# Kernel optimization log

Hardware: AMD Instinct MI355X
Metric: run time of the kernel (lower is better)

The kernel has to match this reference:

```python
import jax, jax.numpy as jnp
import numpy as np

N_NODES = 100000
N_EDGES = 1250000
D_IN = 64
D_OUT = 64


def setup_inputs() -> dict:
    key = jax.random.key(0)
    k_h, k_e, k_src, k_dst, k_w, k_b = jax.random.split(key, 6)
    h = jax.random.normal(k_h, (N_NODES, D_IN), dtype=jnp.float32)
    e = jax.random.normal(k_e, (N_EDGES, 1), dtype=jnp.float32)
    src = jax.random.randint(k_src, (N_EDGES,), 0, N_NODES, dtype=jnp.int64)
    dst = jax.random.randint(k_dst, (N_EDGES,), 0, N_NODES, dtype=jnp.int64)
    W = jax.random.normal(k_w, (D_OUT, D_IN), dtype=jnp.float32) / np.sqrt(D_IN)
    b = jax.random.normal(k_b, (D_OUT,), dtype=jnp.float32) * 0.01
    return {"h": h, "e": e, "src": src, "dst": dst, "W": W, "b": b}


def reference(h, e, src, dst, W, b):
    # u_mul_e: gather source node features and multiply by edge features [E,1] -> [E,D]
    m = h[src] * e
    # fn.sum('m','ft'): scatter-add messages into destination nodes -> [N,D]
    ft = jax.ops.segment_sum(m, dst, num_segments=N_NODES)
    # nn.Linear(input_dim, output_dim)
    return ft @ W.T + b
```

## Files before the change

kernel.cpp:

```cpp
#include <hip/hip_runtime.h>

#define N_NODES 100000
#define N_EDGES 1250000
#define D 64
#define BUCKET_BITS 6
#define BUCKET_SZ 64
#define NBUCK 1563
#define CAP 1024
#define EPT 8
#define EPB (EPT * 256)
#define BIN_BLOCKS ((N_EDGES + EPB - 1) / EPB)


typedef __attribute__((ext_vector_type(8))) short bf16x8;
typedef __attribute__((ext_vector_type(4))) float f32x4;

__device__ __forceinline__ unsigned bf16_rne(float x) {
    unsigned u = __float_as_uint(x);
    return (u + 0x7FFFu + ((u >> 16) & 1u)) >> 16;
}
__device__ __forceinline__ float bf16_to_f(unsigned short v) {
    return __uint_as_float(((unsigned)v) << 16);
}

__device__ __forceinline__ void bf16_split(float x, short& hi, short& lo) {
    unsigned hb = bf16_rne(x);
    float fh = __uint_as_float(hb << 16);
    hi = (short)hb;
    lo = (short)bf16_rne(x - fh);
}

__global__ __launch_bounds__(256) void transform_kernel(const float* __restrict__ h,
                                                        const float* __restrict__ W,
                                                        unsigned short* __restrict__ g16) {
    int t = threadIdx.x;
    int lane = t & 63;
    int w = t >> 6;
    int li = lane & 15;
    int lg = lane >> 4;
    int nodebase = blockIdx.x * 64 + w * 16;

    bf16x8 bhi[4][2], blo[4][2];
#pragma unroll
    for (int nt = 0; nt < 4; ++nt) {
#pragma unroll
        for (int kk = 0; kk < 2; ++kk) {
            const float* wp = W + (nt * 16 + li) * D + kk * 32 + lg * 8;
            float4 w0 = *(const float4*)wp;
            float4 w1 = *(const float4*)(wp + 4);
            float v[8] = {w0.x, w0.y, w0.z, w0.w, w1.x, w1.y, w1.z, w1.w};
            bf16x8 h8, l8;
#pragma unroll
            for (int e = 0; e < 8; ++e) { short a, b; bf16_split(v[e], a, b); h8[e] = a; l8[e] = b; }
            bhi[nt][kk] = h8;
            blo[nt][kk] = l8;
        }
    }

    int arow = nodebase + li;
    if (arow > N_NODES - 1) arow = N_NODES - 1;
    bf16x8 ahi[2], alo[2];
#pragma unroll
    for (int kk = 0; kk < 2; ++kk) {
        const float* hp = h + (long)arow * D + kk * 32 + lg * 8;
        float4 h0 = *(const float4*)hp;
        float4 h1 = *(const float4*)(hp + 4);
        float v[8] = {h0.x, h0.y, h0.z, h0.w, h1.x, h1.y, h1.z, h1.w};
        bf16x8 h8, l8;
#pragma unroll
        for (int e = 0; e < 8; ++e) { short a, b; bf16_split(v[e], a, b); h8[e] = a; l8[e] = b; }
        ahi[kk] = h8;
        alo[kk] = l8;
    }

    f32x4 acc[4];
#pragma unroll
    for (int nt = 0; nt < 4; ++nt) acc[nt] = (f32x4){0.f, 0.f, 0.f, 0.f};
#pragma unroll
    for (int kk = 0; kk < 2; ++kk) {
#pragma unroll
        for (int nt = 0; nt < 4; ++nt) {
            acc[nt] = __builtin_amdgcn_mfma_f32_16x16x32_bf16(ahi[kk], bhi[nt][kk], acc[nt], 0, 0, 0);
            acc[nt] = __builtin_amdgcn_mfma_f32_16x16x32_bf16(ahi[kk], blo[nt][kk], acc[nt], 0, 0, 0);
            acc[nt] = __builtin_amdgcn_mfma_f32_16x16x32_bf16(alo[kk], bhi[nt][kk], acc[nt], 0, 0, 0);
        }
    }

#pragma unroll
    for (int nt = 0; nt < 4; ++nt) {
#pragma unroll
        for (int r = 0; r < 4; ++r) {
            int n = nodebase + lg * 4 + r;
            if (n < N_NODES) g16[(long)n * D + nt * 16 + li] = (unsigned short)bf16_rne(acc[nt][r]);
        }
    }
}

__global__ __launch_bounds__(256) void bin_edges_kernel(const int* __restrict__ src,
                                                        const int* __restrict__ dst,
                                                        const float* __restrict__ e,
                                                        int* __restrict__ gcursor,
                                                        int2* __restrict__ packed) {
    __shared__ int lhist[NBUCK];
    int t = threadIdx.x;
    for (int j = t; j < NBUCK; j += 256) lhist[j] = 0;
    __syncthreads();

    int b[EPT], r[EPT], sv[EPT];
    float ev[EPT];
    int base = blockIdx.x * EPB;
#pragma unroll
    for (int j = 0; j < EPT; ++j) {
        int i = base + j * 256 + t;
        b[j] = -1;
        if (i < N_EDGES) {
            int d = dst[i];
            b[j] = d >> BUCKET_BITS;
            sv[j] = src[i] | ((d & (BUCKET_SZ - 1)) << 20);
            ev[j] = e[i];
            r[j] = atomicAdd(&lhist[b[j]], 1);
        }
    }
    __syncthreads();

    for (int x = t; x < NBUCK; x += 256) {
        int c = lhist[x];
        lhist[x] = (c > 0) ? atomicAdd(&gcursor[x], c) : 0;
    }
    __syncthreads();

#pragma unroll
    for (int j = 0; j < EPT; ++j) {
        if (b[j] >= 0) {
            int pos = lhist[b[j]] + r[j];
            if (pos < CAP) packed[b[j] * CAP + pos] = make_int2(sv[j], __float_as_int(ev[j]));
        }
    }
}

__global__ __launch_bounds__(256) void gather_bucket_kernel(const unsigned short* __restrict__ g16,
                                                            const int2* __restrict__ packed,
                                                            const int* __restrict__ gcursor,
                                                            const float* __restrict__ bias,
                                                            float* __restrict__ out) {
    __shared__ int2 eds[CAP];
    __shared__ int nhist[BUCKET_SZ];
    __shared__ int nbase[BUCKET_SZ];
    __shared__ int ncur[BUCKET_SZ];
    __shared__ int tmp[BUCKET_SZ];

    int t = threadIdx.x;
    int bk = blockIdx.x;
    int start = bk * CAP;
    int cnt = gcursor[bk];
    if (cnt > CAP) cnt = CAP;

    if (t < BUCKET_SZ) nhist[t] = 0;
    __syncthreads();

    for (int i = t; i < cnt; i += 256) {
        int2 p = packed[start + i];
        atomicAdd(&nhist[(p.x >> 20) & (BUCKET_SZ - 1)], 1);
    }
    __syncthreads();

    if (t < BUCKET_SZ) tmp[t] = nhist[t];
    __syncthreads();
#pragma unroll
    for (int off = 1; off < BUCKET_SZ; off <<= 1) {
        int x = 0;
        if (t < BUCKET_SZ && t >= off) x = tmp[t - off];
        __syncthreads();
        if (t < BUCKET_SZ) tmp[t] += x;
        __syncthreads();
    }
    if (t < BUCKET_SZ) {
        int s = tmp[t] - nhist[t];
        nbase[t] = s;
        ncur[t] = s;
    }
    __syncthreads();

    for (int i = t; i < cnt; i += 256) {
        int2 p = packed[start + i];
        int dl = (p.x >> 20) & (BUCKET_SZ - 1);
        int pos = atomicAdd(&ncur[dl], 1);
        eds[pos] = p;
    }
    __syncthreads();

    int w = t >> 6;
    int lane = t & 63;
    float bv = bias[lane];
    for (int jj = 0; jj < 16; ++jj) {
        int n = w * 16 + jj;
        int gn = bk * BUCKET_SZ + n;
        int s = nbase[n];
        int c = nhist[n];
        float acc = bv;
        int k = 0;
        for (; k + 4 <= c; k += 4) {
            int2 p0 = eds[s + k];
            int2 p1 = eds[s + k + 1];
            int2 p2 = eds[s + k + 2];
            int2 p3 = eds[s + k + 3];
            float g0 = bf16_to_f(g16[(p0.x & 0xFFFFF) * D + lane]);
            float g1 = bf16_to_f(g16[(p1.x & 0xFFFFF) * D + lane]);
            float g2 = bf16_to_f(g16[(p2.x & 0xFFFFF) * D + lane]);
            float g3 = bf16_to_f(g16[(p3.x & 0xFFFFF) * D + lane]);
            acc += __int_as_float(p0.y) * g0;
            acc += __int_as_float(p1.y) * g1;
            acc += __int_as_float(p2.y) * g2;
            acc += __int_as_float(p3.y) * g3;
        }
        for (; k < c; ++k) {
            int2 p = eds[s + k];
            acc += __int_as_float(p.y) * bf16_to_f(g16[(p.x & 0xFFFFF) * D + lane]);
        }
        if (gn < N_NODES) out[gn * D + lane] = acc;
    }
}

extern "C" void kernel_launch(void* const* d_in, const int* in_sizes, int n_in,
                              void* d_out, int out_size, void* d_ws, size_t ws_size,
                              hipStream_t stream) {
    const float* h   = (const float*)d_in[0];
    const float* e   = (const float*)d_in[1];
    const int*   src = (const int*)d_in[2];
    const int*   dst = (const int*)d_in[3];
    const float* W   = (const float*)d_in[4];
    const float* b   = (const float*)d_in[5];
    float* out = (float*)d_out;

    char* ws = (char*)d_ws;
    int2*           packed  = (int2*)          (ws);
    int*            gcursor = (int*)           (ws + 12804096);
    unsigned short* g16     = (unsigned short*)(ws + 12810368);

    transform_kernel<<<(N_NODES + 63) / 64, 256, 0, stream>>>(h, W, g16);

    hipMemsetAsync(gcursor, 0, NBUCK * sizeof(int), stream);
    bin_edges_kernel<<<BIN_BLOCKS, 256, 0, stream>>>(src, dst, e, gcursor, packed);

    gather_bucket_kernel<<<NBUCK, 256, 0, stream>>>(g16, packed, gcursor, b, out);
}
```

Before: 174.9 us.

## Replace per-bucket local sort with shared-memory atomic accumulation in gather

The gather kernel no longer counts, prefix-scans and reorders each bucket's edges in shared memory. Each wave now takes a contiguous quarter of the bucket's edges and atomically adds the weighted messages into a 64x64 shared accumulator, which removes several block-wide barriers and passes over the packed edges. The changeset also folds the gcursor memset into the transform kernel, stages the transform output through shared memory so it is written as 16-byte stores, and doubles the edges per thread in the binning kernel. The cost is contention on LDS float atomics and a summation order that is no longer deterministic.

```diff
diff --git a/kernel.cpp b/kernel.cpp
--- a/kernel.cpp
+++ b/kernel.cpp
@@ -7,7 +7,7 @@
 #define BUCKET_SZ 64
 #define NBUCK 1563
 #define CAP 1024
-#define EPT 8
+#define EPT 16
 #define EPB (EPT * 256)
 #define BIN_BLOCKS ((N_EDGES + EPB - 1) / EPB)
 
@@ -32,8 +32,16 @@
 
 __global__ __launch_bounds__(256) void transform_kernel(const float* __restrict__ h,
                                                         const float* __restrict__ W,
-                                                        unsigned short* __restrict__ g16) {
+                                                        unsigned short* __restrict__ g16,
+                                                        int* __restrict__ gcursor) {
+    __shared__ unsigned short sh[64 * D];
+
     int t = threadIdx.x;
+    if (blockIdx.x < 7) {
+        int i = blockIdx.x * 256 + t;
+        if (i < NBUCK) gcursor[i] = 0;
+    }
+
     int lane = t & 63;
     int w = t >> 6;
     int li = lane & 15;
@@ -90,9 +98,17 @@
     for (int nt = 0; nt < 4; ++nt) {
 #pragma unroll
         for (int r = 0; r < 4; ++r) {
-            int n = nodebase + lg * 4 + r;
-            if (n < N_NODES) g16[(long)n * D + nt * 16 + li] = (unsigned short)bf16_rne(acc[nt][r]);
-        }
+            sh[(w * 16 + lg * 4 + r) * D + nt * 16 + li] = (unsigned short)bf16_rne(acc[nt][r]);
+        }
+    }
+    __syncthreads();
+
+    const uint4* s4 = (const uint4*)sh;
+    uint4* g4 = (uint4*)(g16 + (long)blockIdx.x * 64 * D);
+#pragma unroll
+    for (int i = t; i < 512; i += 256) {
+        int n = blockIdx.x * 64 + (i >> 3);
+        if (n < N_NODES) g4[i] = s4[i];
     }
 }
 
@@ -143,81 +159,51 @@
                                                             const int* __restrict__ gcursor,
                                                             const float* __restrict__ bias,
                                                             float* __restrict__ out) {
-    __shared__ int2 eds[CAP];
-    __shared__ int nhist[BUCKET_SZ];
-    __shared__ int nbase[BUCKET_SZ];
-    __shared__ int ncur[BUCKET_SZ];
-    __shared__ int tmp[BUCKET_SZ];
+    __shared__ float acc[BUCKET_SZ][D];
 
     int t = threadIdx.x;
     int bk = blockIdx.x;
-    int start = bk * CAP;
+    int w = t >> 6;
+    int lane = t & 63;
+
+    float4* az = (float4*)acc;
+#pragma unroll
+    for (int i = t; i < 1024; i += 256) az[i] = make_float4(0.f, 0.f, 0.f, 0.f);
+
     int cnt = gcursor[bk];
     if (cnt > CAP) cnt = CAP;
-
-    if (t < BUCKET_SZ) nhist[t] = 0;
-    __syncthreads();
-
-    for (int i = t; i < cnt; i += 256) {
-        int2 p = packed[start + i];
-        atomicAdd(&nhist[(p.x >> 20) & (BUCKET_SZ - 1)], 1);
-    }
-    __syncthreads();
-
-    if (t < BUCKET_SZ) tmp[t] = nhist[t];
-    __syncthreads();
-#pragma unroll
-    for (int off = 1; off < BUCKET_SZ; off <<= 1) {
-        int x = 0;
-        if (t < BUCKET_SZ && t >= off) x = tmp[t - off];
-        __syncthreads();
-        if (t < BUCKET_SZ) tmp[t] += x;
-        __syncthreads();
-    }
-    if (t < BUCKET_SZ) {
-        int s = tmp[t] - nhist[t];
-        nbase[t] = s;
-        ncur[t] = s;
-    }
-    __syncthreads();
-
-    for (int i = t; i < cnt; i += 256) {
-        int2 p = packed[start + i];
-        int dl = (p.x >> 20) & (BUCKET_SZ - 1);
-        int pos = atomicAdd(&ncur[dl], 1);
-        eds[pos] = p;
-    }
-    __syncthreads();
-
-    int w = t >> 6;
-    int lane = t & 63;
+    __syncthreads();
+
+    const int2* pk = packed + bk * CAP;
+    int q = (cnt + 3) >> 2;
+    int s = w * q;
+    int e_ = s + q;
+    if (e_ > cnt) e_ = cnt;
+
+    int k = s;
+    for (; k + 8 <= e_; k += 8) {
+        int2 p[8];
+        float g[8];
+#pragma unroll
+        for (int u = 0; u < 8; ++u) p[u] = pk[k + u];
+#pragma unroll
+        for (int u = 0; u < 8; ++u) g[u] = bf16_to_f(g16[(long)(p[u].x & 0xFFFFF) * D + lane]);
+#pragma unroll
+        for (int u = 0; u < 8; ++u)
+            atomicAdd(&acc[(p[u].x >> 20) & (BUCKET_SZ - 1)][lane], __int_as_float(p[u].y) * g[u]);
+    }
+    for (; k < e_; ++k) {
+        int2 p = pk[k];
+        float g = bf16_to_f(g16[(long)(p.x & 0xFFFFF) * D + lane]);
+        atomicAdd(&acc[(p.x >> 20) & (BUCKET_SZ - 1)][lane], __int_as_float(p.y) * g);
+    }
+    __syncthreads();
+
     float bv = bias[lane];
-    for (int jj = 0; jj < 16; ++jj) {
-        int n = w * 16 + jj;
-        int gn = bk * BUCKET_SZ + n;
-        int s = nbase[n];
-        int c = nhist[n];
-        float acc = bv;
-        int k = 0;
-        for (; k + 4 <= c; k += 4) {
-            int2 p0 = eds[s + k];
-            int2 p1 = eds[s + k + 1];
-            int2 p2 = eds[s + k + 2];
-            int2 p3 = eds[s + k + 3];
-            float g0 = bf16_to_f(g16[(p0.x & 0xFFFFF) * D + lane]);
-            float g1 = bf16_to_f(g16[(p1.x & 0xFFFFF) * D + lane]);
-            float g2 = bf16_to_f(g16[(p2.x & 0xFFFFF) * D + lane]);
-            float g3 = bf16_to_f(g16[(p3.x & 0xFFFFF) * D + lane]);
-            acc += __int_as_float(p0.y) * g0;
-            acc += __int_as_float(p1.y) * g1;
-            acc += __int_as_float(p2.y) * g2;
-            acc += __int_as_float(p3.y) * g3;
-        }
-        for (; k < c; ++k) {
-            int2 p = eds[s + k];
-            acc += __int_as_float(p.y) * bf16_to_f(g16[(p.x & 0xFFFFF) * D + lane]);
-        }
-        if (gn < N_NODES) out[gn * D + lane] = acc;
+#pragma unroll
+    for (int r = w; r < BUCKET_SZ; r += 4) {
+        int gn = bk * BUCKET_SZ + r;
+        if (gn < N_NODES) out[(long)gn * D + lane] = acc[r][lane] + bv;
     }
 }
 
@@ -237,9 +223,8 @@
     int*            gcursor = (int*)           (ws + 12804096);
     unsigned short* g16     = (unsigned short*)(ws + 12810368);
 
-    transform_kernel<<<(N_NODES + 63) / 64, 256, 0, stream>>>(h, W, g16);
-
-    hipMemsetAsync(gcursor, 0, NBUCK * sizeof(int), stream);
+    transform_kernel<<<(N_NODES + 63) / 64, 256, 0, stream>>>(h, W, g16, gcursor);
+
     bin_edges_kernel<<<BIN_BLOCKS, 256, 0, stream>>>(src, dst, e, gcursor, packed);
 
     gather_bucket_kernel<<<NBUCK, 256, 0, stream>>>(g16, packed, gcursor, b, out);
```

Measured after the change: 590.7 us. 3.38x slower.
